# Optimization experiments

Measured on AMD Instinct MI355X. Metric: run time of the kernel, lower is better.

Reference implementation:

```python
import jax, jax.numpy as jnp
import numpy as np

B, T, D, H, BUCKETS = 4, 4096, 1024, 8, 64
DH = D // H          # 128
BSZ = T // BUCKETS   # 64
TEMP = 0.75
SINK_ITERS = 5
LOG_EPS = 1e-6
GUMBEL_EPS = 1e-4


def setup_inputs() -> dict:
    key = jax.random.key(0)
    ks = jax.random.split(key, 6)
    x = jax.random.normal(ks[0], (B, T, D), dtype=jnp.float32)
    w_qkv = jax.random.normal(ks[1], (3 * D, D), dtype=jnp.float32) * 0.02   # torch Linear weight (out,in), no bias
    sort_w = jax.random.normal(ks[2], (1, H, DH, BUCKETS), dtype=jnp.float32)
    w_out = jax.random.normal(ks[3], (D, D), dtype=jnp.float32) * 0.02
    b_out = jnp.zeros((D,), dtype=jnp.float32)
    noise_u = jax.random.uniform(ks[4], (B * H, BUCKETS, BUCKETS), dtype=jnp.float32)
    return {"x": x, "w_qkv": w_qkv, "sort_w": sort_w, "w_out": w_out, "b_out": b_out, "noise_u": noise_u}


def reference(x, w_qkv, sort_w, w_out, b_out, noise_u):
    b, t, d = x.shape
    # qkv projection + merge heads -> (b*h, t, d_h)
    qkv = x @ w_qkv.T
    q, k, v = jnp.split(qkv, 3, axis=2)
    mh = lambda u: u.reshape(b, t, H, DH).transpose(0, 2, 1, 3).reshape(b * H, t, DH)
    q, k, v = mh(q), mh(k), mh(v)
    # bucket -> (b*h, buckets, bsz, d_h)
    bk = lambda u: u.reshape(b * H, BUCKETS, BSZ, DH)
    b_q, b_k, b_v = bk(q), bk(k), bk(v)
    # bucket summaries and sinkhorn sorting matrix R: (b*h, buckets, buckets)
    b_k_r = b_k.sum(axis=2)
    e_w = jnp.broadcast_to(sort_w, (b, H, DH, BUCKETS)).reshape(b * H, DH, BUCKETS)
    R = jnp.log(jax.nn.relu(jnp.einsum('bud,bdv->buv', b_k_r, e_w)) + LOG_EPS)
    gumbel = -jnp.log(-jnp.log(noise_u + GUMBEL_EPS) + GUMBEL_EPS)
    R = (R + gumbel) / TEMP
    for _ in range(SINK_ITERS):
        R = R - jax.nn.logsumexp(R, axis=2, keepdims=True)
        R = R - jax.nn.logsumexp(R, axis=1, keepdims=True)
    R = jnp.tril(jnp.exp(R), k=-1)
    # soft-permute buckets of k and v
    k_re = jnp.einsum('buv,bvtd->butd', R, b_k)
    v_re = jnp.einsum('buv,bvtd->butd', R, b_v)
    b_k2 = jnp.concatenate((k_re, b_k), axis=2)  # (bh, buckets, 2*bsz, dh)
    b_v2 = jnp.concatenate((v_re, b_v), axis=2)
    # bucketed attention (note: scale uses full model dim d, as in source)
    dots = jnp.einsum('buie,buje->buij', b_q, b_k2) * (d ** -0.5)
    attn = jax.nn.softmax(dots, axis=-1)
    out = jnp.einsum('buij,buje->buie', attn, b_v2)
    # unbucket + split heads -> (b, t, d)
    out = out.reshape(b, H, t, DH).transpose(0, 2, 1, 3).reshape(b, t, d)
    return out @ w_out.T + b_out
```

## Files before the change

### kernel.cpp

```cpp
#include <hip/hip_runtime.h>
#include <hip/hip_bf16.h>
#include <cstdint>
#include <cstddef>
#include <math.h>
#include <type_traits>

typedef __bf16 bf16;
typedef __bf16 bf16x4 __attribute__((ext_vector_type(4)));
typedef __bf16 bf16x8 __attribute__((ext_vector_type(8)));
typedef float  f32x4  __attribute__((ext_vector_type(4)));
typedef unsigned u32x2 __attribute__((ext_vector_type(2)));


__device__ inline bool input_is_fp32(const void* x) {
  const unsigned short* u = (const unsigned short*)x;
  const int lane = threadIdx.x & 63;
  const int e = (u[lane] >> 7) & 0xFF;
  return __ballot(e >= 137) != 0ULL;
}

__device__ inline float ldx(const void* p, size_t i, bool f32) {
  return f32 ? ((const float*)p)[i] : (float)((const bf16*)p)[i];
}

template<typename T>
__device__ inline bf16x8 ld8bf(const void* p, size_t i) {
  if constexpr (std::is_same<T, float>::value) {
    const f32x4* q = (const f32x4*)((const float*)p + i);
    const f32x4 a = q[0], b = q[1];
    bf16x8 r;
    r[0]=(bf16)a[0]; r[1]=(bf16)a[1]; r[2]=(bf16)a[2]; r[3]=(bf16)a[3];
    r[4]=(bf16)b[0]; r[5]=(bf16)b[1]; r[6]=(bf16)b[2]; r[7]=(bf16)b[3];
    return r;
  } else {
    return *(const bf16x8*)((const bf16*)p + i);
  }
}

__device__ __forceinline__ void gload16(const void* g, void* l) {
  __builtin_amdgcn_global_load_lds(
      (__attribute__((address_space(1))) void*)g,
      (__attribute__((address_space(3))) void*)l, 16, 0, 0);
}

__global__ __launch_bounds__(256)
void convert_to_bf16(const void* __restrict__ src, bf16* __restrict__ dst,
                     const void* __restrict__ xdet) {
  const bool f32 = input_is_fp32(xdet);
  const size_t i = ((size_t)blockIdx.x * 256 + threadIdx.x) * 8;
  if (f32) *(bf16x8*)&dst[i] = ld8bf<float>(src, i);
  else     *(bf16x8*)&dst[i] = ld8bf<bf16 >(src, i);
}

__global__ __launch_bounds__(256)
void convert_pair(const void* __restrict__ s1, bf16* __restrict__ d1,
                  const void* __restrict__ s2, bf16* __restrict__ d2,
                  const void* __restrict__ xdet) {
  const bool f32 = input_is_fp32(xdet);
  const size_t b = blockIdx.x;
  if (b < 8192) {
    const size_t i = (b*256 + threadIdx.x) * 8;
    if (f32) *(bf16x8*)&d1[i] = ld8bf<float>(s1, i);
    else     *(bf16x8*)&d1[i] = ld8bf<bf16 >(s1, i);
  } else {
    const size_t i = ((b - 8192)*256 + threadIdx.x) * 8;
    if (f32) *(bf16x8*)&d2[i] = ld8bf<float>(s2, i);
    else     *(bf16x8*)&d2[i] = ld8bf<bf16 >(s2, i);
  }
}

template<int EPI>
__global__ __launch_bounds__(512, 2)
void gemm256(const bf16* __restrict__ A, const bf16* __restrict__ Bm,
             const void* __restrict__ bias,
             void* __restrict__ C0, bf16* __restrict__ C1, bf16* __restrict__ C2,
             const void* __restrict__ xdet, int M, int N, int K)
{
  __shared__ __align__(16) bf16 lds[2][2][2][8192];
  const int tid = threadIdx.x, wave = tid >> 6, lane = tid & 63;
  const int fr = lane & 15, quad = lane >> 4;
  const int nwg = gridDim.x * gridDim.y;
  const int cpx = nwg >> 3;
  const int bid = blockIdx.y * gridDim.x + blockIdx.x;
  const int swz = (bid & 7) * cpx + (bid >> 3);
  const int m0 = (swz / gridDim.x) * 256, n0 = (swz % gridDim.x) * 256;
  const int wm = wave >> 2, wn = wave & 3;
  const int gsz  = (quad ^ ((fr >> 1) & 3)) * 16;
  const int srow = wave * 32 + (lane >> 2);
  const int sg   = ((lane & 3) ^ ((lane >> 3) & 3)) * 8;
  const int NT = K >> 6;
  char* ldsb = (char*)&lds[0][0][0][0];

  auto stageA = [&](int buf, int kh, int t) {
    const bf16* s = A + (size_t)(m0 + srow) * K + t*64 + kh*32 + sg;
    char* d = ldsb + buf*65536 + kh*16384 + wave*2048;
    gload16(s, d);
    gload16(s + (size_t)16 * K, d + 1024);
  };
  auto stageB = [&](int buf, int kh, int t) {
    const bf16* s = Bm + (size_t)(n0 + srow) * K + t*64 + kh*32 + sg;
    char* d = ldsb + buf*65536 + 32768 + kh*16384 + wave*2048;
    gload16(s, d);
    gload16(s + (size_t)16 * K, d + 1024);
  };
  auto lda = [&](int c, int kh, int fi) {
    return *(const bf16x8*)(ldsb + c*65536 + kh*16384 + (wm*128 + fi*16 + fr)*64 + gsz);
  };
  auto ldb = [&](int c, int kh, int fi) {
    return *(const bf16x8*)(ldsb + c*65536 + 32768 + kh*16384 + (wn*64 + fi*16 + fr)*64 + gsz);
  };

  f32x4 acc[8][4];
  #pragma unroll
  for (int a = 0; a < 8; ++a)
    #pragma unroll
    for (int b = 0; b < 4; ++b) { f32x4 z = {0.f,0.f,0.f,0.f}; acc[a][b] = z; }

  bf16x8 A0[4], A1[4], B0[4], B1[4];

  stageA(0, 0, 0); stageB(0, 0, 0);
  stageA(0, 1, 0); stageB(0, 1, 0);
  stageA(1, 0, 1); stageB(1, 0, 1);
  asm volatile("s_waitcnt vmcnt(4)" ::: "memory");
  __builtin_amdgcn_s_barrier();

  #pragma unroll 1
  for (int t = 0; t < NT; ++t) {
    const int c = t & 1;
    const bool d12 = (t + 1 < NT), d34 = (t + 2 < NT);

    #pragma unroll
    for (int n = 0; n < 4; ++n) B0[n] = ldb(c, 0, n);
    #pragma unroll
    for (int m = 0; m < 4; ++m) A0[m] = lda(c, 0, m);
    #pragma unroll
    for (int m = 0; m < 4; ++m) A1[m] = lda(c, 0, 4 + m);
    if (d12) stageA(c ^ 1, 1, t + 1);
    __builtin_amdgcn_s_barrier();
    asm volatile("s_waitcnt lgkmcnt(4)" ::: "memory");
    __builtin_amdgcn_sched_barrier(0);
    __builtin_amdgcn_s_setprio(1);
    #pragma unroll
    for (int m = 0; m < 4; ++m)
      #pragma unroll
      for (int n = 0; n < 4; ++n)
        acc[m][n] = __builtin_amdgcn_mfma_f32_16x16x32_bf16(A0[m], B0[n], acc[m][n], 0, 0, 0);
    __builtin_amdgcn_s_setprio(0);
    __builtin_amdgcn_s_barrier();

    if (d12) stageB(c ^ 1, 1, t + 1);
    __builtin_amdgcn_s_barrier();
    asm volatile("s_waitcnt lgkmcnt(0)" ::: "memory");
    __builtin_amdgcn_sched_barrier(0);
    __builtin_amdgcn_s_setprio(1);
    #pragma unroll
    for (int m = 0; m < 4; ++m)
      #pragma unroll
      for (int n = 0; n < 4; ++n)
        acc[4 + m][n] = __builtin_amdgcn_mfma_f32_16x16x32_bf16(A1[m], B0[n], acc[4 + m][n], 0, 0, 0);
    __builtin_amdgcn_s_setprio(0);
    __builtin_amdgcn_s_barrier();

    #pragma unroll
    for (int n = 0; n < 4; ++n) B1[n] = ldb(c, 1, n);
    #pragma unroll
    for (int m = 0; m < 4; ++m) A0[m] = lda(c, 1, m);
    #pragma unroll
    for (int m = 0; m < 4; ++m) A1[m] = lda(c, 1, 4 + m);
    if (d34) stageA(c, 0, t + 2);
    __builtin_amdgcn_s_barrier();
    asm volatile("s_waitcnt lgkmcnt(4)" ::: "memory");
    __builtin_amdgcn_sched_barrier(0);
    __builtin_amdgcn_s_setprio(1);
    #pragma unroll
    for (int m = 0; m < 4; ++m)
      #pragma unroll
      for (int n = 0; n < 4; ++n)
        acc[m][n] = __builtin_amdgcn_mfma_f32_16x16x32_bf16(A0[m], B1[n], acc[m][n], 0, 0, 0);
    __builtin_amdgcn_s_setprio(0);
    __builtin_amdgcn_s_barrier();

    if (d34) stageB(c, 0, t + 2);
    __builtin_amdgcn_s_barrier();
    asm volatile("s_waitcnt lgkmcnt(0)" ::: "memory");
    __builtin_amdgcn_sched_barrier(0);
    __builtin_amdgcn_s_setprio(1);
    #pragma unroll
    for (int m = 0; m < 4; ++m)
      #pragma unroll
      for (int n = 0; n < 4; ++n)
        acc[4 + m][n] = __builtin_amdgcn_mfma_f32_16x16x32_bf16(A1[m], B1[n], acc[4 + m][n], 0, 0, 0);
    __builtin_amdgcn_s_setprio(0);
    if (t < NT - 2)       { asm volatile("s_waitcnt vmcnt(4)" ::: "memory"); }
    else if (t == NT - 2) { asm volatile("s_waitcnt vmcnt(0)" ::: "memory"); }
    __builtin_amdgcn_s_barrier();
  }

  if constexpr (EPI == 0) {
    const int sel = n0 >> 10;
    const int cb  = (n0 & 1023) + wn * 64;
    #pragma unroll
    for (int im = 0; im < 8; ++im) {
      const int mrow = m0 + wm*128 + im*16 + quad*4;
      const int b = mrow >> 12, tt = mrow & 4095;
      const int u = tt >> 6, i = tt & 63;
      #pragma unroll
      for (int nn = 0; nn < 4; ++nn) {
        const int cc = cb + nn*16 + fr;
        const int h = cc >> 7, e = cc & 127;
        const size_t bhu = (size_t)((b*8 + h)*64 + u);
        if (sel == 2) {
          bf16x4 w;
          #pragma unroll
          for (int r = 0; r < 4; ++r) w[r] = (bf16)acc[im][nn][r];
          *(bf16x4*)&C2[(bhu*128 + e)*64 + i] = w;
        } else {
          bf16* dst = (sel == 0) ? (bf16*)C0 : C1;
          #pragma unroll
          for (int r = 0; r < 4; ++r)
            dst[(bhu*64 + i + r)*128 + e] = (bf16)acc[im][nn][r];
        }
      }
    }
  } else {
    const bool f32o = input_is_fp32(xdet);
    #pragma unroll
    for (int im = 0; im < 8; ++im) {
      #pragma unroll
      for (int nn = 0; nn < 4; ++nn) {
        #pragma unroll
        for (int r = 0; r < 4; ++r) {
          const int m = m0 + wm*128 + im*16 + quad*4 + r;
          const int n = n0 + wn*64 + nn*16 + fr;
          const float val = acc[im][nn][r] + ldx(bias, n, f32o);
          if (f32o) ((float*)C0)[(size_t)m*N + n] = val;
          else      ((bf16*)C0)[(size_t)m*N + n] = (bf16)val;
        }
      }
    }
  }
}

__global__ __launch_bounds__(128)
void bksum(const bf16* __restrict__ k_ws, float* __restrict__ bkr_g)
{
  const int ug = blockIdx.x, bh = blockIdx.y, t = threadIdx.x;
  const int ul = t >> 4, e0 = (t & 15) * 8;
  const int u = ug * 8 + ul;
  const bf16* p = k_ws + ((size_t)bh*64 + u)*8192 + e0;
  float acc[8];
  #pragma unroll
  for (int j = 0; j < 8; ++j) acc[j] = 0.f;
  for (int i = 0; i < 64; ++i) {
    bf16x8 kv = *(const bf16x8*)&p[i*128];
    #pragma unroll
    for (int j = 0; j < 8; ++j) acc[j] += (float)kv[j];
  }
  float* dst = bkr_g + (size_t)bh*8192 + u*128 + e0;
  #pragma unroll
  for (int j = 0; j < 8; ++j) dst[j] = acc[j];
}

__global__ __launch_bounds__(256)
void sinkhorn_R(const float* __restrict__ bkr_g, const void* __restrict__ sort_w,
                const void* __restrict__ noise, float* __restrict__ R_buf,
                const void* __restrict__ xdet)
{
  const bool f32 = input_is_fp32(xdet);
  const int bh = blockIdx.x, h = bh & 7, tid = threadIdx.x;
  __shared__ float bkr[64*128];
  __shared__ float ew[128*64];
  __shared__ float R[64*65];

  for (int f = tid; f < 64*128; f += 256) bkr[f] = bkr_g[(size_t)bh*8192 + f];
  for (int f = tid; f < 128*64; f += 256) ew[f] = ldx(sort_w, (size_t)h*8192 + f, f32);
  __syncthreads();

  for (int f = tid; f < 64*64; f += 256) {
    const int u = f >> 6, v = f & 63;
    float s = 0.f;
    for (int e = 0; e < 128; ++e) s += bkr[u*128 + e] * ew[e*64 + v];
    s = fmaxf(s, 0.f);
    const float r  = logf(s + 1e-6f);
    const double nz = (double)ldx(noise, ((size_t)bh*64 + u)*64 + v, f32);
    const double t1 = log(nz + 1e-4);
    const double t2 = fmax(-t1 + 1e-4, 1e-30);
    const float g = (float)(-log(t2));
    R[u*65 + v] = (r + g) * (1.f / 0.75f);
  }
  __syncthreads();

  const int rc = tid >> 2, c4 = tid & 3;
  for (int it = 0; it < 5; ++it) {
    {
      float mx = -1e30f;
      for (int v = c4; v < 64; v += 4) mx = fmaxf(mx, R[rc*65 + v]);
      mx = fmaxf(mx, __shfl_xor(mx, 1));
      mx = fmaxf(mx, __shfl_xor(mx, 2));
      float s = 0.f;
      for (int v = c4; v < 64; v += 4) s += expf(R[rc*65 + v] - mx);
      s += __shfl_xor(s, 1);
      s += __shfl_xor(s, 2);
      const float l = mx + logf(s);
      for (int v = c4; v < 64; v += 4) R[rc*65 + v] -= l;
    }
    __syncthreads();
    {
      float mx = -1e30f;
      for (int u = c4; u < 64; u += 4) mx = fmaxf(mx, R[u*65 + rc]);
      mx = fmaxf(mx, __shfl_xor(mx, 1));
      mx = fmaxf(mx, __shfl_xor(mx, 2));
      float s = 0.f;
      for (int u = c4; u < 64; u += 4) s += expf(R[u*65 + rc] - mx);
      s += __shfl_xor(s, 1);
      s += __shfl_xor(s, 2);
      const float l = mx + logf(s);
      for (int u = c4; u < 64; u += 4) R[u*65 + rc] -= l;
    }
    __syncthreads();
  }

  for (int f = tid; f < 64*64; f += 256) {
    const int u = f >> 6, v = f & 63;
    R_buf[(size_t)bh*4096 + f] = (u > v) ? expf(R[u*65 + v]) : 0.f;
  }
}

__global__ __launch_bounds__(256)
void permute_kv(const float* __restrict__ R_buf,
                const bf16* __restrict__ Xk, const bf16* __restrict__ Xv,
                bf16* __restrict__ Ok, bf16* __restrict__ Ov, int bh0)
{
  const int tid = threadIdx.x;
  const int bhl = blockIdx.y, bh = bh0 + bhl;
  const int f0  = blockIdx.x * 256;
  const bf16* X = blockIdx.z ? Xv : Xk;
  bf16*       O = blockIdx.z ? Ov : Ok;

  __shared__ __align__(16) bf16 A_lds[64*136];
  __shared__ __align__(16) bf16 X_lds[16*1048];

  {
    const bf16* Xg = X + (size_t)bh*524288 + f0;
    const int vb = tid >> 5, c = tid & 31;
    const int dst = (c >> 1)*1048 + (c & 1)*8;
    #pragma unroll
    for (int p = 0; p < 8; ++p) {
      const int v = vb + p*8;
      *(bf16x8*)&X_lds[dst + v*16] = *(const bf16x8*)&Xg[(size_t)v*8192 + c*8];
    }
  }
  {
    const float* Rg = R_buf + (size_t)bh*4096;
    #pragma unroll
    for (int p = 0; p < 16; ++p) {
      const int idx = tid + p*256;
      const int uu = idx >> 6, vv = idx & 63;
      const float r = Rg[idx];
      const bf16 hi = (bf16)r;
      const float lo = r - (float)hi;
      A_lds[uu*136 + vv]      = hi;
      A_lds[uu*136 + 64 + vv] = (bf16)lo;
    }
  }
  __syncthreads();

  const int lane = tid & 63, wave = tid >> 6;
  const int fr = lane & 15, quad = lane >> 4;

  bf16x8 af[4][4];
  #pragma unroll
  for (int mt = 0; mt < 4; ++mt)
    #pragma unroll
    for (int ks = 0; ks < 4; ++ks)
      af[mt][ks] = *(const bf16x8*)&A_lds[(mt*16 + fr)*136 + ks*32 + quad*8];

  f32x4 acc[4][4];
  #pragma unroll
  for (int a = 0; a < 4; ++a)
    #pragma unroll
    for (int b = 0; b < 4; ++b) { f32x4 z = {0.f,0.f,0.f,0.f}; acc[a][b] = z; }

  #pragma unroll
  for (int nt = 0; nt < 4; ++nt) {
    const int g = wave*4 + nt;
    const unsigned addr = (unsigned)(size_t)
        (__attribute__((address_space(3))) bf16*)&X_lds[g*1048 + quad*128 + fr*4];
    u32x2 p0, p1, p2, p3;
    asm volatile(
      "ds_read_b64_tr_b16 %0, %4\n"
      "ds_read_b64_tr_b16 %1, %4 offset:128\n"
      "ds_read_b64_tr_b16 %2, %4 offset:1024\n"
      "ds_read_b64_tr_b16 %3, %4 offset:1152\n"
      : "=&v"(p0), "=&v"(p1), "=&v"(p2), "=&v"(p3)
      : "v"(addr));
    asm volatile("s_waitcnt lgkmcnt(0)" ::: "memory");
    __builtin_amdgcn_sched_barrier(0);
    union { u32x2 u[2]; bf16x8 v; } c0, c1;
    c0.u[0] = p0; c0.u[1] = p1;
    c1.u[0] = p2; c1.u[1] = p3;
    const bf16x8 b0 = c0.v, b1 = c1.v;
    #pragma unroll
    for (int mt = 0; mt < 4; ++mt) {
      acc[mt][nt] = __builtin_amdgcn_mfma_f32_16x16x32_bf16(af[mt][0], b0, acc[mt][nt], 0, 0, 0);
      acc[mt][nt] = __builtin_amdgcn_mfma_f32_16x16x32_bf16(af[mt][1], b1, acc[mt][nt], 0, 0, 0);
      acc[mt][nt] = __builtin_amdgcn_mfma_f32_16x16x32_bf16(af[mt][2], b0, acc[mt][nt], 0, 0, 0);
      acc[mt][nt] = __builtin_amdgcn_mfma_f32_16x16x32_bf16(af[mt][3], b1, acc[mt][nt], 0, 0, 0);
    }
  }

  bf16* Og = O + (size_t)bhl*524288 + f0;
  #pragma unroll
  for (int mt = 0; mt < 4; ++mt)
    #pragma unroll
    for (int nt = 0; nt < 4; ++nt)
      #pragma unroll
      for (int r = 0; r < 4; ++r)
        Og[(size_t)(mt*16 + quad*4 + r)*8192 + wave*64 + nt*16 + fr] = (bf16)acc[mt][nt][r];
}

__global__ __launch_bounds__(256)
void attn_mfma(const bf16* __restrict__ q_ws, const bf16* __restrict__ k_ws,
               const bf16* __restrict__ vT_ws,
               const bf16* __restrict__ kre_g, const bf16* __restrict__ vre_g,
               bf16* __restrict__ aout, int bh0)
{
  const int u = blockIdx.x, bhl = blockIdx.y, bh = bh0 + bhl;
  const int tid = threadIdx.x;
  const int lane = tid & 63, wave = tid >> 6;
  const int fr = lane & 15, quad = lane >> 4;

  __shared__ __align__(16) unsigned char smem[34048];
  float* sc = (float*)smem;
  bf16*  pA = (bf16*)smem;

  const size_t tileq = ((size_t)bh *64 + u) * 8192;
  const size_t tilel = ((size_t)bhl*64 + u) * 8192;

  bf16x8 pvT[2][2];
  #pragma unroll
  for (int nt = 0; nt < 2; ++nt) {
    const int e = wave*32 + nt*16 + fr;
    #pragma unroll
    for (int k2 = 0; k2 < 2; ++k2)
      pvT[nt][k2] = *(const bf16x8*)&vT_ws[tileq + (size_t)e*64 + k2*32 + quad*8];
  }

  {
    f32x4 dacc[4][2];
    #pragma unroll
    for (int mt = 0; mt < 4; ++mt)
      #pragma unroll
      for (int nt = 0; nt < 2; ++nt) { f32x4 z = {0.f,0.f,0.f,0.f}; dacc[mt][nt] = z; }
    #pragma unroll
    for (int ks = 0; ks < 4; ++ks) {
      bf16x8 afr[4];
      #pragma unroll
      for (int mt = 0; mt < 4; ++mt)
        afr[mt] = *(const bf16x8*)&q_ws[tileq + (size_t)(mt*16 + fr)*128 + ks*32 + quad*8];
      #pragma unroll
      for (int nt = 0; nt < 2; ++nt) {
        const int j = wave*32 + nt*16 + fr;
        bf16x8 bfr;
        if (wave < 2) bfr = *(const bf16x8*)&kre_g[tilel + (size_t)j*128 + ks*32 + quad*8];
        else          bfr = *(const bf16x8*)&k_ws[tileq + (size_t)(j - 64)*128 + ks*32 + quad*8];
        #pragma unroll
        for (int mt = 0; mt < 4; ++mt)
          dacc[mt][nt] = __builtin_amdgcn_mfma_f32_16x16x32_bf16(afr[mt], bfr, dacc[mt][nt], 0, 0, 0);
      }
    }
    #pragma unroll
    for (int mt = 0; mt < 4; ++mt)
      #pragma unroll
      for (int nt = 0; nt < 2; ++nt)
        #pragma unroll
        for (int r = 0; r < 4; ++r)
          sc[(mt*16 + quad*4 + r)*132 + wave*32 + nt*16 + fr] = dacc[mt][nt][r] * 0.03125f;
  }
  __syncthreads();

  {
    const int i = tid >> 2, jc = tid & 3;
    float pv[32];
    float mx = -1e30f;
    #pragma unroll
    for (int t = 0; t < 32; ++t) { pv[t] = sc[i*132 + jc + t*4]; mx = fmaxf(mx, pv[t]); }
    mx = fmaxf(mx, __shfl_xor(mx, 1));
    mx = fmaxf(mx, __shfl_xor(mx, 2));
    float s = 0.f;
    #pragma unroll
    for (int t = 0; t < 32; ++t) { pv[t] = expf(pv[t] - mx); s += pv[t]; }
    s += __shfl_xor(s, 1);
    s += __shfl_xor(s, 2);
    const float inv = 1.f / s;
    __syncthreads();
    #pragma unroll
    for (int t = 0; t < 32; ++t) pA[i*136 + jc + t*4] = (bf16)(pv[t] * inv);
  }
  __syncthreads();

  {
    f32x4 oacc[4][2];
    #pragma unroll
    for (int mt = 0; mt < 4; ++mt)
      #pragma unroll
      for (int nt = 0; nt < 2; ++nt) { f32x4 z = {0.f,0.f,0.f,0.f}; oacc[mt][nt] = z; }
    #pragma unroll
    for (int ks = 0; ks < 4; ++ks) {
      bf16x8 afr[4];
      #pragma unroll
      for (int mt = 0; mt < 4; ++mt)
        afr[mt] = *(const bf16x8*)&pA[(mt*16 + fr)*136 + ks*32 + quad*8];
      #pragma unroll
      for (int nt = 0; nt < 2; ++nt) {
        bf16x8 bfr;
        if (ks < 2) {
          const int e = wave*32 + nt*16 + fr;
          bfr = *(const bf16x8*)&vre_g[tilel + (size_t)e*64 + ks*32 + quad*8];
        } else {
          bfr = pvT[nt][ks - 2];
        }
        #pragma unroll
        for (int mt = 0; mt < 4; ++mt)
          oacc[mt][nt] = __builtin_amdgcn_mfma_f32_16x16x32_bf16(afr[mt], bfr, oacc[mt][nt], 0, 0, 0);
      }
    }
    __syncthreads();
    #pragma unroll
    for (int mt = 0; mt < 4; ++mt)
      #pragma unroll
      for (int nt = 0; nt < 2; ++nt)
        #pragma unroll
        for (int r = 0; r < 4; ++r)
          pA[(mt*16 + quad*4 + r)*136 + wave*32 + nt*16 + fr] = (bf16)oacc[mt][nt][r];
  }
  __syncthreads();

  {
    const int b = bh >> 3, h = bh & 7;
    #pragma unroll
    for (int r = 0; r < 4; ++r) {
      const int f = r*2048 + tid*8;
      const int i = f >> 7, e0 = f & 127;
      bf16x8 w = *(const bf16x8*)&pA[i*136 + e0];
      *(bf16x8*)&aout[((size_t)(b*4096 + u*64 + i))*1024 + h*128 + e0] = w;
    }
  }
}

extern "C" void kernel_launch(void* const* d_in, const int* in_sizes, int n_in,
                              void* d_out, int out_size, void* d_ws, size_t ws_size,
                              hipStream_t stream)
{
  (void)in_sizes; (void)n_in; (void)out_size; (void)ws_size;
  const void* x      = d_in[0];
  const void* w_qkv  = d_in[1];
  const void* sort_w = d_in[2];
  const void* w_out  = d_in[3];
  const void* b_out  = d_in[4];
  const void* noise  = d_in[5];

  char* ws = (char*)d_ws;
  const size_t TEN = (size_t)32*64*64*128;
  const size_t HEN = TEN / 2;
  bf16* q_ws  = (bf16*)ws;
  bf16* k_ws  = q_ws + TEN;
  bf16* vT_ws = k_ws + TEN;
  bf16* xa_ws = vT_ws + TEN;

  float* bkr_g = (float*)((char*)xa_ws + (size_t)30*1024*1024);
  float* R_buf = (float*)((char*)xa_ws + (size_t)31*1024*1024);
  bf16* wqkv_bf = (bf16*)((char*)d_out + (1536<<10));
  bf16* kre = (bf16*)d_out;
  bf16* vre = kre + HEN;
  bf16* wout_bf = k_ws;

  convert_pair<<<9728, 256, 0, stream>>>(x, xa_ws, w_qkv, wqkv_bf, x);

  gemm256<0><<<dim3(12,64), 512, 0, stream>>>(xa_ws, wqkv_bf, nullptr,
                                              q_ws, k_ws, vT_ws, x, 16384, 3072, 1024);

  bksum<<<dim3(8,32), 128, 0, stream>>>(k_ws, bkr_g);
  sinkhorn_R<<<32, 256, 0, stream>>>(bkr_g, sort_w, noise, R_buf, x);

  permute_kv<<<dim3(32,16,2), 256, 0, stream>>>(R_buf, k_ws, vT_ws, kre, vre, 0);
  attn_mfma<<<dim3(64,16), 256, 0, stream>>>(q_ws, k_ws, vT_ws, kre, vre, xa_ws, 0);
  permute_kv<<<dim3(32,16,2), 256, 0, stream>>>(R_buf, k_ws, vT_ws, kre, vre, 16);
  attn_mfma<<<dim3(64,16), 256, 0, stream>>>(q_ws, k_ws, vT_ws, kre, vre, xa_ws, 16);

  convert_to_bf16<<<512, 256, 0, stream>>>(w_out, wout_bf, x);
  gemm256<1><<<dim3(4,64), 512, 0, stream>>>(xa_ws, wout_bf, b_out,
                                             d_out, nullptr, nullptr, x, 16384, 1024, 1024);
}
```

Measured before the change: 424.4 us.

## Shrink GEMM tile to 256x128 with K-step 32 and raise occupancy

Rewrites the shared GEMM kernel to use 256x128 output tiles and a 32-wide K step with a simpler two-buffer pipeline, instead of 256x256 tiles with 64-wide K. LDS drops to 48KB and per-thread accumulators halve, and launch bounds now ask for 4 workgroups per CU. The grids double so there are more workgroups to spread over CUs. The trade-off is lower arithmetic intensity per tile and twice as many K iterations and barriers, and the new schedule no longer interleaves staging with the MFMA phases.

```diff
diff --git a/kernel.cpp b/kernel.cpp
--- a/kernel.cpp
+++ b/kernel.cpp
@@ -70,128 +70,84 @@
 }
 
 template<int EPI>
-__global__ __launch_bounds__(512, 2)
+__global__ __launch_bounds__(512, 4)
 void gemm256(const bf16* __restrict__ A, const bf16* __restrict__ Bm,
              const void* __restrict__ bias,
              void* __restrict__ C0, bf16* __restrict__ C1, bf16* __restrict__ C2,
              const void* __restrict__ xdet, int M, int N, int K)
 {
-  __shared__ __align__(16) bf16 lds[2][2][2][8192];
+  __shared__ __align__(16) bf16 lds[2][12288];
   const int tid = threadIdx.x, wave = tid >> 6, lane = tid & 63;
   const int fr = lane & 15, quad = lane >> 4;
   const int nwg = gridDim.x * gridDim.y;
   const int cpx = nwg >> 3;
   const int bid = blockIdx.y * gridDim.x + blockIdx.x;
   const int swz = (bid & 7) * cpx + (bid >> 3);
-  const int m0 = (swz / gridDim.x) * 256, n0 = (swz % gridDim.x) * 256;
-  const int wm = wave >> 2, wn = wave & 3;
-  const int gsz  = (quad ^ ((fr >> 1) & 3)) * 16;
-  const int srow = wave * 32 + (lane >> 2);
-  const int sg   = ((lane & 3) ^ ((lane >> 3) & 3)) * 8;
-  const int NT = K >> 6;
-  char* ldsb = (char*)&lds[0][0][0][0];
-
-  auto stageA = [&](int buf, int kh, int t) {
-    const bf16* s = A + (size_t)(m0 + srow) * K + t*64 + kh*32 + sg;
-    char* d = ldsb + buf*65536 + kh*16384 + wave*2048;
+  const int m0 = (swz / gridDim.x) * 256, n0 = (swz % gridDim.x) * 128;
+  const int wm = wave >> 1, wn = wave & 1;
+  const int gsz = (quad ^ ((fr >> 1) & 3)) * 16;
+  const int sg  = ((lane & 3) ^ ((lane >> 3) & 3)) * 8;
+  const int NT = K >> 5;
+  char* ldsb = (char*)&lds[0][0];
+
+  auto stageA = [&](int buf, int t) {
+    const bf16* s = A + (size_t)(m0 + wave*32 + (lane >> 2)) * K + t*32 + sg;
+    char* d = ldsb + buf*24576 + wave*2048;
     gload16(s, d);
     gload16(s + (size_t)16 * K, d + 1024);
   };
-  auto stageB = [&](int buf, int kh, int t) {
-    const bf16* s = Bm + (size_t)(n0 + srow) * K + t*64 + kh*32 + sg;
-    char* d = ldsb + buf*65536 + 32768 + kh*16384 + wave*2048;
+  auto stageB = [&](int buf, int t) {
+    const bf16* s = Bm + (size_t)(n0 + wave*16 + (lane >> 2)) * K + t*32 + sg;
+    char* d = ldsb + buf*24576 + 16384 + wave*1024;
     gload16(s, d);
-    gload16(s + (size_t)16 * K, d + 1024);
   };
-  auto lda = [&](int c, int kh, int fi) {
-    return *(const bf16x8*)(ldsb + c*65536 + kh*16384 + (wm*128 + fi*16 + fr)*64 + gsz);
+  auto lda = [&](int c, int fi) {
+    return *(const bf16x8*)(ldsb + c*24576 + (wm*64 + fi*16 + fr)*64 + gsz);
   };
-  auto ldb = [&](int c, int kh, int fi) {
-    return *(const bf16x8*)(ldsb + c*65536 + 32768 + kh*16384 + (wn*64 + fi*16 + fr)*64 + gsz);
+  auto ldb = [&](int c, int fi) {
+    return *(const bf16x8*)(ldsb + c*24576 + 16384 + (wn*64 + fi*16 + fr)*64 + gsz);
   };
 
-  f32x4 acc[8][4];
-  #pragma unroll
-  for (int a = 0; a < 8; ++a)
+  f32x4 acc[4][4];
+  #pragma unroll
+  for (int a = 0; a < 4; ++a)
     #pragma unroll
     for (int b = 0; b < 4; ++b) { f32x4 z = {0.f,0.f,0.f,0.f}; acc[a][b] = z; }
 
-  bf16x8 A0[4], A1[4], B0[4], B1[4];
-
-  stageA(0, 0, 0); stageB(0, 0, 0);
-  stageA(0, 1, 0); stageB(0, 1, 0);
-  stageA(1, 0, 1); stageB(1, 0, 1);
-  asm volatile("s_waitcnt vmcnt(4)" ::: "memory");
+  stageA(0, 0); stageB(0, 0);
+  stageA(1, 1); stageB(1, 1);
+  asm volatile("s_waitcnt vmcnt(3)" ::: "memory");
   __builtin_amdgcn_s_barrier();
 
   #pragma unroll 1
   for (int t = 0; t < NT; ++t) {
     const int c = t & 1;
-    const bool d12 = (t + 1 < NT), d34 = (t + 2 < NT);
-
-    #pragma unroll
-    for (int n = 0; n < 4; ++n) B0[n] = ldb(c, 0, n);
-    #pragma unroll
-    for (int m = 0; m < 4; ++m) A0[m] = lda(c, 0, m);
-    #pragma unroll
-    for (int m = 0; m < 4; ++m) A1[m] = lda(c, 0, 4 + m);
-    if (d12) stageA(c ^ 1, 1, t + 1);
-    __builtin_amdgcn_s_barrier();
-    asm volatile("s_waitcnt lgkmcnt(4)" ::: "memory");
+    bf16x8 Af[4], Bf[4];
+    #pragma unroll
+    for (int n = 0; n < 4; ++n) Bf[n] = ldb(c, n);
+    #pragma unroll
+    for (int m = 0; m < 4; ++m) Af[m] = lda(c, m);
+    asm volatile("s_waitcnt lgkmcnt(2)" ::: "memory");
     __builtin_amdgcn_sched_barrier(0);
     __builtin_amdgcn_s_setprio(1);
     #pragma unroll
-    for (int m = 0; m < 4; ++m)
+    for (int m = 0; m < 2; ++m)
       #pragma unroll
       for (int n = 0; n < 4; ++n)
-        acc[m][n] = __builtin_amdgcn_mfma_f32_16x16x32_bf16(A0[m], B0[n], acc[m][n], 0, 0, 0);
+        acc[m][n] = __builtin_amdgcn_mfma_f32_16x16x32_bf16(Af[m], Bf[n], acc[m][n], 0, 0, 0);
     __builtin_amdgcn_s_setprio(0);
-    __builtin_amdgcn_s_barrier();
-
-    if (d12) stageB(c ^ 1, 1, t + 1);
-    __builtin_amdgcn_s_barrier();
     asm volatile("s_waitcnt lgkmcnt(0)" ::: "memory");
     __builtin_amdgcn_sched_barrier(0);
     __builtin_amdgcn_s_setprio(1);
     #pragma unroll
-    for (int m = 0; m < 4; ++m)
+    for (int m = 2; m < 4; ++m)
       #pragma unroll
       for (int n = 0; n < 4; ++n)
-        acc[4 + m][n] = __builtin_amdgcn_mfma_f32_16x16x32_bf16(A1[m], B0[n], acc[4 + m][n], 0, 0, 0);
+        acc[m][n] = __builtin_amdgcn_mfma_f32_16x16x32_bf16(Af[m], Bf[n], acc[m][n], 0, 0, 0);
     __builtin_amdgcn_s_setprio(0);
     __builtin_amdgcn_s_barrier();
-
-    #pragma unroll
-    for (int n = 0; n < 4; ++n) B1[n] = ldb(c, 1, n);
-    #pragma unroll
-    for (int m = 0; m < 4; ++m) A0[m] = lda(c, 1, m);
-    #pragma unroll
-    for (int m = 0; m < 4; ++m) A1[m] = lda(c, 1, 4 + m);
-    if (d34) stageA(c, 0, t + 2);
-    __builtin_amdgcn_s_barrier();
-    asm volatile("s_waitcnt lgkmcnt(4)" ::: "memory");
-    __builtin_amdgcn_sched_barrier(0);
-    __builtin_amdgcn_s_setprio(1);
-    #pragma unroll
-    for (int m = 0; m < 4; ++m)
-      #pragma unroll
-      for (int n = 0; n < 4; ++n)
-        acc[m][n] = __builtin_amdgcn_mfma_f32_16x16x32_bf16(A0[m], B1[n], acc[m][n], 0, 0, 0);
-    __builtin_amdgcn_s_setprio(0);
-    __builtin_amdgcn_s_barrier();
-
-    if (d34) stageB(c, 0, t + 2);
-    __builtin_amdgcn_s_barrier();
-    asm volatile("s_waitcnt lgkmcnt(0)" ::: "memory");
-    __builtin_amdgcn_sched_barrier(0);
-    __builtin_amdgcn_s_setprio(1);
-    #pragma unroll
-    for (int m = 0; m < 4; ++m)
-      #pragma unroll
-      for (int n = 0; n < 4; ++n)
-        acc[4 + m][n] = __builtin_amdgcn_mfma_f32_16x16x32_bf16(A1[m], B1[n], acc[4 + m][n], 0, 0, 0);
-    __builtin_amdgcn_s_setprio(0);
-    if (t < NT - 2)       { asm volatile("s_waitcnt vmcnt(4)" ::: "memory"); }
+    if (t + 2 < NT) { stageA(c, t + 2); stageB(c, t + 2); }
+    if (t < NT - 2)       { asm volatile("s_waitcnt vmcnt(3)" ::: "memory"); }
     else if (t == NT - 2) { asm volatile("s_waitcnt vmcnt(0)" ::: "memory"); }
     __builtin_amdgcn_s_barrier();
   }
@@ -200,8 +156,8 @@
     const int sel = n0 >> 10;
     const int cb  = (n0 & 1023) + wn * 64;
     #pragma unroll
-    for (int im = 0; im < 8; ++im) {
-      const int mrow = m0 + wm*128 + im*16 + quad*4;
+    for (int im = 0; im < 4; ++im) {
+      const int mrow = m0 + wm*64 + im*16 + quad*4;
       const int b = mrow >> 12, tt = mrow & 4095;
       const int u = tt >> 6, i = tt & 63;
       #pragma unroll
@@ -225,12 +181,12 @@
   } else {
     const bool f32o = input_is_fp32(xdet);
     #pragma unroll
-    for (int im = 0; im < 8; ++im) {
+    for (int im = 0; im < 4; ++im) {
       #pragma unroll
       for (int nn = 0; nn < 4; ++nn) {
         #pragma unroll
         for (int r = 0; r < 4; ++r) {
-          const int m = m0 + wm*128 + im*16 + quad*4 + r;
+          const int m = m0 + wm*64 + im*16 + quad*4 + r;
           const int n = n0 + wn*64 + nn*16 + fr;
           const float val = acc[im][nn][r] + ldx(bias, n, f32o);
           if (f32o) ((float*)C0)[(size_t)m*N + n] = val;
@@ -577,7 +533,7 @@
 
   convert_pair<<<9728, 256, 0, stream>>>(x, xa_ws, w_qkv, wqkv_bf, x);
 
-  gemm256<0><<<dim3(12,64), 512, 0, stream>>>(xa_ws, wqkv_bf, nullptr,
+  gemm256<0><<<dim3(24,64), 512, 0, stream>>>(xa_ws, wqkv_bf, nullptr,
                                               q_ws, k_ws, vT_ws, x, 16384, 3072, 1024);
 
   bksum<<<dim3(8,32), 128, 0, stream>>>(k_ws, bkr_g);
@@ -589,6 +545,6 @@
   attn_mfma<<<dim3(64,16), 256, 0, stream>>>(q_ws, k_ws, vT_ws, kre, vre, xa_ws, 16);
 
   convert_to_bf16<<<512, 256, 0, stream>>>(w_out, wout_bf, x);
-  gemm256<1><<<dim3(4,64), 512, 0, stream>>>(xa_ws, wout_bf, b_out,
+  gemm256<1><<<dim3(8,64), 512, 0, stream>>>(xa_ws, wout_bf, b_out,
                                              d_out, nullptr, nullptr, x, 16384, 1024, 1024);
 }
```

New measurement: 422.9 us. Within noise of the previous version (-0.4%).
